# Performance work log

Measured on AMD Instinct MI355X. Metric: run time of the kernel, lower is better.

Reference implementation:

```python
import jax, jax.numpy as jnp
import numpy as np
from jax import lax


def setup_inputs() -> dict:
    key = jax.random.key(0)
    k1, k2, k3, k4, k5 = jax.random.split(key, 5)
    B, C_in, H, W = 32768, 3, 14, 14
    C_out, kh, kw = 16, 5, 5
    num_outputs = 1000
    return {
        "feature_map": jax.random.normal(k1, (B, C_in, H, W), dtype=jnp.float32),
        "conv_w": jax.random.normal(k2, (C_out, C_in, kh, kw), dtype=jnp.float32),
        "conv_b": jax.random.normal(k3, (C_out,), dtype=jnp.float32),
        "lin_w": jax.random.normal(k4, (num_outputs, C_out * 5 * 5), dtype=jnp.float32),
        "lin_b": jax.random.normal(k5, (num_outputs,), dtype=jnp.float32),
    }


def reference(feature_map, conv_w, conv_b, lin_w, lin_b):
    # Conv2D: valid cross-correlation, stride 1, no padding (B,Ci,H,W)x(Co,Ci,h,w)->(B,Co,H-h+1,W-w+1)
    y = lax.conv_general_dilated(
        feature_map, conv_w, window_strides=(1, 1), padding="VALID",
        dimension_numbers=("NCHW", "OIHW", "NCHW"))
    y = jax.nn.relu(y + conv_b[None, :, None, None])
    # Non-overlapping 2x2 max pool: (B,C,10,10) -> (B,C,5,5)
    B, C, H, W = y.shape
    y = y.reshape(B, C, H // 2, 2, W // 2, 2).max(axis=(3, 5))
    # Linear head on flattened features (B, C*5*5) -> (B, num_outputs)
    out = y.reshape(B, -1) @ lin_w.T + lin_b
    return out
```

## Files before the change

### kernel.cpp

```cpp
#include <hip/hip_runtime.h>
#include <stdint.h>

#define BTOT 32768
#define NIMG 16
#define KF   416

typedef __attribute__((ext_vector_type(8))) short short8;
typedef __attribute__((ext_vector_type(4))) float floatx4;

__device__ __forceinline__ unsigned short f2bf(float x) {
    union { float f; unsigned int u; } v; v.f = x;
    unsigned int r = v.u + 0x7fffu + ((v.u >> 16) & 1u);
    return (unsigned short)(r >> 16);
}

__global__ __launch_bounds__(256) void conv_pool_kernel(
    const float* __restrict__ fm, const float* __restrict__ cw,
    const float* __restrict__ cb, unsigned short* __restrict__ feat,
    const float* __restrict__ lw, unsigned short* __restrict__ Wb)
{
    if (blockIdx.x >= BTOT / NIMG) {
        int c = (blockIdx.x - BTOT / NIMG) * 256 + threadIdx.x;
        if (c < 1024 * 52) {
            int n = c / 52;
            int kc = (c - n * 52) * 8;
            unsigned short v[8];
            #pragma unroll
            for (int j = 0; j < 8; ++j) {
                int k = kc + j;
                float x = (n < 1000 && k < 400) ? lw[n * 400 + k] : 0.f;
                v[j] = f2bf(x);
            }
            *(uint4*)(Wb + (size_t)n * KF + kc) = *(uint4*)v;
        }
        return;
    }

    __shared__ __align__(16) unsigned short s_img[NIMG * 588];
    __shared__ __align__(16) unsigned short s_out[NIMG * 416];

    const int tid  = threadIdx.x;
    const int b0   = blockIdx.x * NIMG;
    const int lane = tid & 63;
    const int wave = tid >> 6;

    const float4* in4 = (const float4*)(fm + (size_t)b0 * 588);
    for (int idx = tid; idx < NIMG * 147 / 2; idx += 256) {
        float4 v0 = in4[2 * idx], v1 = in4[2 * idx + 1];
        uint4 u;
        u.x = (unsigned int)f2bf(v0.x) | ((unsigned int)f2bf(v0.y) << 16);
        u.y = (unsigned int)f2bf(v0.z) | ((unsigned int)f2bf(v0.w) << 16);
        u.z = (unsigned int)f2bf(v1.x) | ((unsigned int)f2bf(v1.y) << 16);
        u.w = (unsigned int)f2bf(v1.z) | ((unsigned int)f2bf(v1.w) << 16);
        *(uint4*)&s_img[idx * 8] = u;
    }
    {
        int img = tid >> 4, k = tid & 15;
        s_out[img * 416 + 400 + k] = 0;
    }

    const int co = lane & 15;
    const int q  = lane >> 4;
    const int r  = lane & 15;
    const int qd = r >> 2;
    const int cy = (r >> 1) & 1;
    const int cx = r & 1;
    const int sh = cx << 4;

    union U8 { unsigned short h[8]; short8 v; };
    U8 bw[4];
    int chunkdw[4];
    #pragma unroll
    for (int i = 0; i < 4; ++i) {
        int c = 4 * i + q;
        int ci = (c < 15) ? (c / 5) : 0;
        int row = (c < 15) ? (c - ci * 5) : 0;
        chunkdw[i] = ci * 98 + row * 7;
        #pragma unroll
        for (int j = 0; j < 8; ++j)
            bw[i].h[j] = (c < 15 && j < 5) ? f2bf(cw[co * 75 + ci * 25 + row * 5 + j])
                                           : (unsigned short)0;
    }
    const float bias = cb[co];

    __syncthreads();

    const unsigned int* sw32 = (const unsigned int*)s_img + wave * 1176;
    unsigned short* ow = s_out + wave * 4 * 416;

    for (int t = 0; t < 25; ++t) {
        int g   = t * 4 + qd;
        int img = (g * 41) >> 10;
        int q25 = g - img * 25;
        int qy  = (q25 * 13) >> 6;
        int qx  = q25 - qy * 5;
        int wb  = img * 294 + (qy * 2 + cy) * 7 + qx;

        floatx4 acc = {0.f, 0.f, 0.f, 0.f};
        #pragma unroll
        for (int i = 0; i < 4; ++i) {
            const unsigned int* p = sw32 + wb + chunkdw[i];
            unsigned int d0 = p[0], d1 = p[1], d2 = p[2];
            union { unsigned int u[4]; short8 v; } a;
            a.u[0] = __builtin_amdgcn_alignbit(d1, d0, sh);
            a.u[1] = __builtin_amdgcn_alignbit(d2, d1, sh);
            a.u[2] = __builtin_amdgcn_alignbit(d2, d2, sh);
            a.u[3] = 0;
            acc = __builtin_amdgcn_mfma_f32_16x16x32_bf16(a.v, bw[i].v, acc, 0, 0, 0);
        }

        int gd   = t * 4 + q;
        int imgd = (gd * 41) >> 10;
        int q25d = gd - imgd * 25;
        float m = fmaxf(fmaxf(acc[0], acc[1]), fmaxf(acc[2], acc[3])) + bias;
        ow[imgd * 416 + co * 25 + q25d] = f2bf(fmaxf(m, 0.f));
    }

    __syncthreads();
    const uint4* so4 = (const uint4*)s_out;
    uint4* fo4 = (uint4*)(feat + (size_t)b0 * KF);
    for (int idx = tid; idx < NIMG * 52; idx += 256)
        fo4[idx] = so4[idx];
}

__global__ __launch_bounds__(256) void gemm_kernel(
    const unsigned short* __restrict__ F, const unsigned short* __restrict__ Wb,
    const float* __restrict__ lb, float* __restrict__ out)
{
    __shared__ __align__(16) unsigned short At[128 * 32];
    __shared__ __align__(16) unsigned short Bt[128 * 32];

    const int tid = threadIdx.x;
    const int bm = blockIdx.x >> 3;
    const int bn = blockIdx.x & 7;
    const int m0 = bm * 128;
    const int n0 = bn * 128;

    const int w = tid >> 6;
    const int lane = tid & 63;
    const int wm = w & 1, wn = w >> 1;
    const int lq = lane >> 4, ln = lane & 15;

    floatx4 zero = {0.f, 0.f, 0.f, 0.f};
    floatx4 acc[4][4];
    #pragma unroll
    for (int i = 0; i < 4; ++i)
        #pragma unroll
        for (int j = 0; j < 4; ++j) acc[i][j] = zero;

    const int srow = w * 16 + (lane >> 2);
    const int skc = (lane & 3) * 8;
    const unsigned short* gA = F + (size_t)(m0 + srow) * KF + skc;
    const unsigned short* gB = Wb + (size_t)(n0 + srow) * KF + skc;

    for (int kb = 0; kb < KF; kb += 32) {
        #pragma unroll
        for (int t = 0; t < 2; ++t) {
            __builtin_amdgcn_global_load_lds(
                (const __attribute__((address_space(1))) void*)(gA + (size_t)(t * 64) * KF + kb),
                (__attribute__((address_space(3))) void*)&At[(w * 16 + t * 64) * 32],
                16, 0, 0);
            __builtin_amdgcn_global_load_lds(
                (const __attribute__((address_space(1))) void*)(gB + (size_t)(t * 64) * KF + kb),
                (__attribute__((address_space(3))) void*)&Bt[(w * 16 + t * 64) * 32],
                16, 0, 0);
        }
        __syncthreads();
        short8 af[4], bf[4];
        #pragma unroll
        for (int i = 0; i < 4; ++i)
            af[i] = *(const short8*)&At[(wm * 64 + i * 16 + ln) * 32 + lq * 8];
        #pragma unroll
        for (int j = 0; j < 4; ++j)
            bf[j] = *(const short8*)&Bt[(wn * 64 + j * 16 + ln) * 32 + lq * 8];
        #pragma unroll
        for (int i = 0; i < 4; ++i)
            #pragma unroll
            for (int j = 0; j < 4; ++j)
                acc[i][j] = __builtin_amdgcn_mfma_f32_16x16x32_bf16(af[i], bf[j], acc[i][j], 0, 0, 0);
        __syncthreads();
    }

    #pragma unroll
    for (int j = 0; j < 4; ++j) {
        int n = n0 + wn * 64 + j * 16 + ln;
        if (n >= 1000) continue;
        float bias = lb[n];
        #pragma unroll
        for (int i = 0; i < 4; ++i) {
            int mb = m0 + wm * 64 + i * 16 + lq * 4;
            #pragma unroll
            for (int rr = 0; rr < 4; ++rr)
                out[(size_t)(mb + rr) * 1000 + n] = acc[i][j][rr] + bias;
        }
    }
}

extern "C" void kernel_launch(void* const* d_in, const int* in_sizes, int n_in,
                              void* d_out, int out_size, void* d_ws, size_t ws_size,
                              hipStream_t stream)
{
    const float* fm = (const float*)d_in[0];
    const float* cw = (const float*)d_in[1];
    const float* cb = (const float*)d_in[2];
    const float* lw = (const float*)d_in[3];
    const float* lb = (const float*)d_in[4];
    float* out = (float*)d_out;

    unsigned short* feat = (unsigned short*)d_ws;
    unsigned short* Wb   = (unsigned short*)d_ws + (size_t)BTOT * KF;

    conv_pool_kernel<<<BTOT / NIMG + 208, 256, 0, stream>>>(fm, cw, cb, feat, lw, Wb);
    gemm_kernel<<<2048, 256, 0, stream>>>(feat, Wb, lb, out);
}
```

Measured before the change: 302.5 us.

## Prefetch conv LDS operands across iterations and write pooled features directly to global

The conv loop is fully unrolled and software-pipelined: the LDS words for the next pooled position are loaded into registers while the current MFMAs run, and the per-iteration div/mod index math becomes incremental counters. The s_out staging buffer, its final block barrier and the coalesced copy-out are removed; each lane stores its bf16 result straight to global, and the K padding is zeroed per wave. This cuts LDS traffic and a sync, but global writes become scattered 2-byte stores, which may be less efficient, and register pressure rises.

```diff
diff --git a/kernel.cpp b/kernel.cpp
--- a/kernel.cpp
+++ b/kernel.cpp
@@ -7,6 +7,7 @@
 
 typedef __attribute__((ext_vector_type(8))) short short8;
 typedef __attribute__((ext_vector_type(4))) float floatx4;
+typedef __attribute__((ext_vector_type(4))) unsigned int uintx4;
 
 __device__ __forceinline__ unsigned short f2bf(float x) {
     union { float f; unsigned int u; } v; v.f = x;
@@ -37,7 +38,6 @@
     }
 
     __shared__ __align__(16) unsigned short s_img[NIMG * 588];
-    __shared__ __align__(16) unsigned short s_out[NIMG * 416];
 
     const int tid  = threadIdx.x;
     const int b0   = blockIdx.x * NIMG;
@@ -54,10 +54,6 @@
         u.w = (unsigned int)f2bf(v1.z) | ((unsigned int)f2bf(v1.w) << 16);
         *(uint4*)&s_img[idx * 8] = u;
     }
-    {
-        int img = tid >> 4, k = tid & 15;
-        s_out[img * 416 + 400 + k] = 0;
-    }
 
     const int co = lane & 15;
     const int q  = lane >> 4;
@@ -67,60 +63,75 @@
     const int cx = r & 1;
     const int sh = cx << 4;
 
-    union U8 { unsigned short h[8]; short8 v; };
-    U8 bw[4];
-    int chunkdw[4];
+    short8 bw[4];
+    int cdw[4];
     #pragma unroll
     for (int i = 0; i < 4; ++i) {
         int c = 4 * i + q;
         int ci = (c < 15) ? (c / 5) : 0;
         int row = (c < 15) ? (c - ci * 5) : 0;
-        chunkdw[i] = ci * 98 + row * 7;
+        cdw[i] = ci * 98 + row * 7;
         #pragma unroll
         for (int j = 0; j < 8; ++j)
-            bw[i].h[j] = (c < 15 && j < 5) ? f2bf(cw[co * 75 + ci * 25 + row * 5 + j])
-                                           : (unsigned short)0;
+            bw[i][j] = (c < 15 && j < 5) ? (short)f2bf(cw[co * 75 + ci * 25 + row * 5 + j])
+                                         : (short)0;
     }
     const float bias = cb[co];
 
     __syncthreads();
 
     const unsigned int* sw32 = (const unsigned int*)s_img + wave * 1176;
-    unsigned short* ow = s_out + wave * 4 * 416;
-
+    unsigned short* fb = feat + (size_t)(b0 + wave * 4) * KF + co * 25;
+
+    int imga = 0, q25a = qd;
+    int imgs = 0, q25s = q;
+
+    unsigned int cur[12], nxt[12];
+
+    {
+        int qy = (q25a * 13) >> 6, qx = q25a - qy * 5;
+        const unsigned int* p = sw32 + imga * 294 + (qy * 2 + cy) * 7 + qx;
+        #pragma unroll
+        for (int i = 0; i < 4; ++i) {
+            cur[3 * i] = p[cdw[i]]; cur[3 * i + 1] = p[cdw[i] + 1]; cur[3 * i + 2] = p[cdw[i] + 2];
+        }
+    }
+
+    #pragma unroll
     for (int t = 0; t < 25; ++t) {
-        int g   = t * 4 + qd;
-        int img = (g * 41) >> 10;
-        int q25 = g - img * 25;
-        int qy  = (q25 * 13) >> 6;
-        int qx  = q25 - qy * 5;
-        int wb  = img * 294 + (qy * 2 + cy) * 7 + qx;
-
+        if (t < 24) {
+            q25a += 4; if (q25a >= 25) { q25a -= 25; imga += 1; }
+            int qy = (q25a * 13) >> 6, qx = q25a - qy * 5;
+            const unsigned int* p = sw32 + imga * 294 + (qy * 2 + cy) * 7 + qx;
+            #pragma unroll
+            for (int i = 0; i < 4; ++i) {
+                nxt[3 * i] = p[cdw[i]]; nxt[3 * i + 1] = p[cdw[i] + 1]; nxt[3 * i + 2] = p[cdw[i] + 2];
+            }
+        }
         floatx4 acc = {0.f, 0.f, 0.f, 0.f};
         #pragma unroll
         for (int i = 0; i < 4; ++i) {
-            const unsigned int* p = sw32 + wb + chunkdw[i];
-            unsigned int d0 = p[0], d1 = p[1], d2 = p[2];
-            union { unsigned int u[4]; short8 v; } a;
-            a.u[0] = __builtin_amdgcn_alignbit(d1, d0, sh);
-            a.u[1] = __builtin_amdgcn_alignbit(d2, d1, sh);
-            a.u[2] = __builtin_amdgcn_alignbit(d2, d2, sh);
-            a.u[3] = 0;
-            acc = __builtin_amdgcn_mfma_f32_16x16x32_bf16(a.v, bw[i].v, acc, 0, 0, 0);
-        }
-
-        int gd   = t * 4 + q;
-        int imgd = (gd * 41) >> 10;
-        int q25d = gd - imgd * 25;
+            uintx4 a;
+            a.x = __builtin_amdgcn_alignbit(cur[3 * i + 1], cur[3 * i + 0], sh);
+            a.y = __builtin_amdgcn_alignbit(cur[3 * i + 2], cur[3 * i + 1], sh);
+            a.z = __builtin_amdgcn_alignbit(cur[3 * i + 2], cur[3 * i + 2], sh);
+            a.w = 0u;
+            acc = __builtin_amdgcn_mfma_f32_16x16x32_bf16(
+                __builtin_bit_cast(short8, a), bw[i], acc, 0, 0, 0);
+        }
         float m = fmaxf(fmaxf(acc[0], acc[1]), fmaxf(acc[2], acc[3])) + bias;
-        ow[imgd * 416 + co * 25 + q25d] = f2bf(fmaxf(m, 0.f));
-    }
-
-    __syncthreads();
-    const uint4* so4 = (const uint4*)s_out;
-    uint4* fo4 = (uint4*)(feat + (size_t)b0 * KF);
-    for (int idx = tid; idx < NIMG * 52; idx += 256)
-        fo4[idx] = so4[idx];
+        fb[imgs * 416 + q25s] = f2bf(fmaxf(m, 0.f));
+        if (t < 24) {
+            q25s += 4; if (q25s >= 25) { q25s -= 25; imgs += 1; }
+            #pragma unroll
+            for (int k = 0; k < 12; ++k) cur[k] = nxt[k];
+        }
+    }
+
+    if (lane < 16) {
+        int img = lane >> 2, k = lane & 3;
+        *(uint2*)(feat + (size_t)(b0 + wave * 4 + img) * KF + 400 + k * 4) = make_uint2(0u, 0u);
+    }
 }
 
 __global__ __launch_bounds__(256) void gemm_kernel(
```

Result: no change. 303.1 us (+0.2%).

## Remap conv MFMA lanes to images and pool inside accumulators, write features directly

Applied to the files above, without the earlier changes.

Restructures the conv+pool stage so each MFMA row is an image and each column an output channel. The four pooling-window positions are computed as separate accumulators and max-reduced in registers. The LDS output staging buffer and its extra barrier are removed, and pooled bf16 features go straight to global memory as scattered 2-byte stores. The rewrite also cuts per-iteration index arithmetic and lets loaded image words be shared across the shifted-window operands, at the cost of uncoalesced narrow global writes.

```diff
diff --git a/kernel.cpp b/kernel.cpp
--- a/kernel.cpp
+++ b/kernel.cpp
@@ -7,12 +7,22 @@
 
 typedef __attribute__((ext_vector_type(8))) short short8;
 typedef __attribute__((ext_vector_type(4))) float floatx4;
+typedef __attribute__((ext_vector_type(4))) unsigned int uintx4;
 
 __device__ __forceinline__ unsigned short f2bf(float x) {
     union { float f; unsigned int u; } v; v.f = x;
     unsigned int r = v.u + 0x7fffu + ((v.u >> 16) & 1u);
     return (unsigned short)(r >> 16);
 }
+__device__ __forceinline__ unsigned int pk2(float a, float b) {
+    return (unsigned int)f2bf(a) | ((unsigned int)f2bf(b) << 16);
+}
+
+#define MK0(d0, d1, d2) __builtin_bit_cast(short8, (uintx4){(d0), (d1), (d2), (d0)})
+#define MK1(d0, d1, d2) __builtin_bit_cast(short8, (uintx4){ \
+    __builtin_amdgcn_alignbit((d1), (d0), 16), \
+    __builtin_amdgcn_alignbit((d2), (d1), 16), \
+    (d2) >> 16, (d0)})
 
 __global__ __launch_bounds__(256) void conv_pool_kernel(
     const float* __restrict__ fm, const float* __restrict__ cw,
@@ -36,91 +46,106 @@
         return;
     }
 
-    __shared__ __align__(16) unsigned short s_img[NIMG * 588];
-    __shared__ __align__(16) unsigned short s_out[NIMG * 416];
+    __shared__ __align__(16) unsigned int s_img[NIMG * 294];
 
     const int tid  = threadIdx.x;
     const int b0   = blockIdx.x * NIMG;
     const int lane = tid & 63;
-    const int wave = tid >> 6;
 
     const float4* in4 = (const float4*)(fm + (size_t)b0 * 588);
     for (int idx = tid; idx < NIMG * 147 / 2; idx += 256) {
         float4 v0 = in4[2 * idx], v1 = in4[2 * idx + 1];
         uint4 u;
-        u.x = (unsigned int)f2bf(v0.x) | ((unsigned int)f2bf(v0.y) << 16);
-        u.y = (unsigned int)f2bf(v0.z) | ((unsigned int)f2bf(v0.w) << 16);
-        u.z = (unsigned int)f2bf(v1.x) | ((unsigned int)f2bf(v1.y) << 16);
-        u.w = (unsigned int)f2bf(v1.z) | ((unsigned int)f2bf(v1.w) << 16);
-        *(uint4*)&s_img[idx * 8] = u;
+        u.x = pk2(v0.x, v0.y);
+        u.y = pk2(v0.z, v0.w);
+        u.z = pk2(v1.x, v1.y);
+        u.w = pk2(v1.z, v1.w);
+        *(uint4*)&s_img[idx * 4] = u;
     }
     {
         int img = tid >> 4, k = tid & 15;
-        s_out[img * 416 + 400 + k] = 0;
-    }
-
-    const int co = lane & 15;
+        feat[(size_t)(b0 + img) * KF + 400 + k] = 0;
+    }
+
+    const int il = lane & 15;
     const int q  = lane >> 4;
-    const int r  = lane & 15;
-    const int qd = r >> 2;
-    const int cy = (r >> 1) & 1;
-    const int cx = r & 1;
-    const int sh = cx << 4;
-
-    union U8 { unsigned short h[8]; short8 v; };
-    U8 bw[4];
-    int chunkdw[4];
-    #pragma unroll
-    for (int i = 0; i < 4; ++i) {
-        int c = 4 * i + q;
-        int ci = (c < 15) ? (c / 5) : 0;
-        int row = (c < 15) ? (c - ci * 5) : 0;
-        chunkdw[i] = ci * 98 + row * 7;
-        #pragma unroll
-        for (int j = 0; j < 8; ++j)
-            bw[i].h[j] = (c < 15 && j < 5) ? f2bf(cw[co * 75 + ci * 25 + row * 5 + j])
-                                           : (unsigned short)0;
-    }
-    const float bias = cb[co];
+
+    const int o0 = q == 0 ? 0   : q == 1 ? 7   : q == 2 ? 14  : 21;
+    const int o1 = q == 0 ? 28  : q == 1 ? 105 : q == 2 ? 98  : 119;
+    const int o2 = q == 0 ? 112 : q == 1 ? 203 : q == 2 ? 126 : 217;
+    const int o3 = q == 0 ? 196 : q == 1 ? 210 : q == 2 ? 224 : 7;
+
+    auto loadw = [&](int o, bool ph) -> short8 {
+        short8 w = {};
+        if (!ph) {
+            int ci  = o >= 196 ? 2 : (o >= 98 ? 1 : 0);
+            int row = (o - ci * 98) / 7;
+            #pragma unroll
+            for (int j = 0; j < 5; ++j)
+                w[j] = (short)f2bf(cw[il * 75 + ci * 25 + row * 5 + j]);
+        }
+        return w;
+    };
+    const short8 bw0 = loadw(o0, false);
+    const short8 bw1 = loadw(o1, false);
+    const short8 bw2 = loadw(o2, false);
+    const short8 bw3 = loadw(o3, q == 3);
+    const float bias = cb[il];
 
     __syncthreads();
 
-    const unsigned int* sw32 = (const unsigned int*)s_img + wave * 1176;
-    unsigned short* ow = s_out + wave * 4 * 416;
-
-    for (int t = 0; t < 25; ++t) {
-        int g   = t * 4 + qd;
-        int img = (g * 41) >> 10;
-        int q25 = g - img * 25;
-        int qy  = (q25 * 13) >> 6;
-        int qx  = q25 - qy * 5;
-        int wb  = img * 294 + (qy * 2 + cy) * 7 + qx;
-
-        floatx4 acc = {0.f, 0.f, 0.f, 0.f};
-        #pragma unroll
-        for (int i = 0; i < 4; ++i) {
-            const unsigned int* p = sw32 + wb + chunkdw[i];
-            unsigned int d0 = p[0], d1 = p[1], d2 = p[2];
-            union { unsigned int u[4]; short8 v; } a;
-            a.u[0] = __builtin_amdgcn_alignbit(d1, d0, sh);
-            a.u[1] = __builtin_amdgcn_alignbit(d2, d1, sh);
-            a.u[2] = __builtin_amdgcn_alignbit(d2, d2, sh);
-            a.u[3] = 0;
-            acc = __builtin_amdgcn_mfma_f32_16x16x32_bf16(a.v, bw[i].v, acc, 0, 0, 0);
-        }
-
-        int gd   = t * 4 + q;
-        int imgd = (gd * 41) >> 10;
-        int q25d = gd - imgd * 25;
-        float m = fmaxf(fmaxf(acc[0], acc[1]), fmaxf(acc[2], acc[3])) + bias;
-        ow[imgd * 416 + co * 25 + q25d] = f2bf(fmaxf(m, 0.f));
-    }
-
-    __syncthreads();
-    const uint4* so4 = (const uint4*)s_out;
-    uint4* fo4 = (uint4*)(feat + (size_t)b0 * KF);
-    for (int idx = tid; idx < NIMG * 52; idx += 256)
-        fo4[idx] = so4[idx];
+    const unsigned int* ap0 = s_img + il * 294 + o0;
+    const unsigned int* ap1 = s_img + il * 294 + o1;
+    const unsigned int* ap2 = s_img + il * 294 + o2;
+    const unsigned int* ap3 = s_img + il * 294 + o3;
+
+    const int wave = tid >> 6;
+    int p = wave, qy = 0, qx = wave;
+    while (p < 25) {
+        const int u = qy * 14 + qx;
+
+        unsigned int d00 = ap0[u], d01 = ap0[u + 1], d02 = ap0[u + 2];
+        unsigned int d10 = ap1[u], d11 = ap1[u + 1], d12 = ap1[u + 2];
+        unsigned int d20 = ap2[u], d21 = ap2[u + 1], d22 = ap2[u + 2];
+        unsigned int d30 = ap3[u], d31 = ap3[u + 1], d32 = ap3[u + 2];
+        unsigned int e00 = ap0[u + 7], e01 = ap0[u + 8], e02 = ap0[u + 9];
+        unsigned int e10 = ap1[u + 7], e11 = ap1[u + 8], e12 = ap1[u + 9];
+        unsigned int e20 = ap2[u + 7], e21 = ap2[u + 8], e22 = ap2[u + 9];
+        unsigned int e30 = ap3[u + 7], e31 = ap3[u + 8], e32 = ap3[u + 9];
+
+        floatx4 z = {0.f, 0.f, 0.f, 0.f};
+        floatx4 A00 = z, A01 = z, A10 = z, A11 = z;
+
+        A00 = __builtin_amdgcn_mfma_f32_16x16x32_bf16(MK0(d00, d01, d02), bw0, A00, 0, 0, 0);
+        A00 = __builtin_amdgcn_mfma_f32_16x16x32_bf16(MK0(d10, d11, d12), bw1, A00, 0, 0, 0);
+        A00 = __builtin_amdgcn_mfma_f32_16x16x32_bf16(MK0(d20, d21, d22), bw2, A00, 0, 0, 0);
+        A00 = __builtin_amdgcn_mfma_f32_16x16x32_bf16(MK0(d30, d31, d32), bw3, A00, 0, 0, 0);
+
+        A01 = __builtin_amdgcn_mfma_f32_16x16x32_bf16(MK1(d00, d01, d02), bw0, A01, 0, 0, 0);
+        A01 = __builtin_amdgcn_mfma_f32_16x16x32_bf16(MK1(d10, d11, d12), bw1, A01, 0, 0, 0);
+        A01 = __builtin_amdgcn_mfma_f32_16x16x32_bf16(MK1(d20, d21, d22), bw2, A01, 0, 0, 0);
+        A01 = __builtin_amdgcn_mfma_f32_16x16x32_bf16(MK1(d30, d31, d32), bw3, A01, 0, 0, 0);
+
+        A10 = __builtin_amdgcn_mfma_f32_16x16x32_bf16(MK0(e00, e01, e02), bw0, A10, 0, 0, 0);
+        A10 = __builtin_amdgcn_mfma_f32_16x16x32_bf16(MK0(e10, e11, e12), bw1, A10, 0, 0, 0);
+        A10 = __builtin_amdgcn_mfma_f32_16x16x32_bf16(MK0(e20, e21, e22), bw2, A10, 0, 0, 0);
+        A10 = __builtin_amdgcn_mfma_f32_16x16x32_bf16(MK0(e30, e31, e32), bw3, A10, 0, 0, 0);
+
+        A11 = __builtin_amdgcn_mfma_f32_16x16x32_bf16(MK1(e00, e01, e02), bw0, A11, 0, 0, 0);
+        A11 = __builtin_amdgcn_mfma_f32_16x16x32_bf16(MK1(e10, e11, e12), bw1, A11, 0, 0, 0);
+        A11 = __builtin_amdgcn_mfma_f32_16x16x32_bf16(MK1(e20, e21, e22), bw2, A11, 0, 0, 0);
+        A11 = __builtin_amdgcn_mfma_f32_16x16x32_bf16(MK1(e30, e31, e32), bw3, A11, 0, 0, 0);
+
+        unsigned short* fq = feat + (size_t)(b0 + 4 * q) * KF + il * 25 + p;
+        #pragma unroll
+        for (int rr = 0; rr < 4; ++rr) {
+            float m = fmaxf(fmaxf(A00[rr], A01[rr]), fmaxf(A10[rr], A11[rr])) + bias;
+            fq[(size_t)rr * KF] = f2bf(fmaxf(m, 0.f));
+        }
+
+        p += 4; qx += 4;
+        if (qx >= 5) { qx -= 5; ++qy; }
+    }
 }
 
 __global__ __launch_bounds__(256) void gemm_kernel(
```

Result: slower. 323.7 us (+7.0%).
